# Kernel optimization log

Measured on AMD Instinct MI355X. Metric: run time of the kernel, lower is better.

The kernel has to match this reference:

```python
import jax, jax.numpy as jnp
import numpy as np

N_NODES = 50000
N_EDGES = 800000
IN_DIM = 128
HID = 32
HEADS = 8
N_CLASSES = 10
N_GRAPHS = 64
NEG_SLOPE = 0.2


def _lin(key, fan_in, fan_out):
    return jax.random.normal(key, (fan_in, fan_out), jnp.float32) / np.sqrt(fan_in)


def setup_inputs() -> dict:
    key = jax.random.key(0)
    ks = jax.random.split(key, 24)
    x = jax.random.normal(ks[0], (N_NODES, IN_DIM), jnp.float32)
    edge_index = jax.random.randint(ks[1], (2, N_EDGES), 0, N_NODES, jnp.int64)
    batch = jnp.sort(jax.random.randint(ks[2], (N_NODES,), 0, N_GRAPHS, jnp.int64))
    HC = HEADS * HID
    return {
        "x": x,
        "edge_index": edge_index,
        "batch": batch,
        # GATConv(IN_DIM, HID, heads=8): shared lin, att_src/att_dst, bias on concat output
        "gat_W": _lin(ks[3], IN_DIM, HC),
        "gat_att_src": jax.random.normal(ks[4], (HEADS, HID), jnp.float32) / np.sqrt(HID),
        "gat_att_dst": jax.random.normal(ks[5], (HEADS, HID), jnp.float32) / np.sqrt(HID),
        "gat_b": jnp.zeros((HC,), jnp.float32),
        # GraphConv(HC, HID): lin_rel (bias) on aggregated neighbors + lin_root (no bias)
        "W2_rel": _lin(ks[6], HC, HID), "b2": jnp.zeros((HID,), jnp.float32), "W2_root": _lin(ks[7], HC, HID),
        # SAGEConv(HID, HID): lin_l (bias) on mean-aggregated neighbors + lin_r (no bias)
        "W3_l": _lin(ks[8], HID, HID), "b3": jnp.zeros((HID,), jnp.float32), "W3_r": _lin(ks[9], HID, HID),
        # GraphConv(HID, HID)
        "W4_rel": _lin(ks[10], HID, HID), "b4": jnp.zeros((HID,), jnp.float32), "W4_root": _lin(ks[11], HID, HID),
        "fc1_W": _lin(ks[12], HID, HID), "fc1_b": jnp.zeros((HID,), jnp.float32),
        "fc2_W": _lin(ks[13], HID, N_CLASSES), "fc2_b": jnp.zeros((N_CLASSES,), jnp.float32),
    }


def _segment_softmax(logits, seg_ids, num_segments):
    # numerically-stable softmax over edges grouped by destination node
    m = jax.ops.segment_max(logits, seg_ids, num_segments=num_segments)
    e = jnp.exp(logits - m[seg_ids])
    z = jax.ops.segment_sum(e, seg_ids, num_segments=num_segments)
    return e / (z[seg_ids] + 1e-16)


def _gnn_forward(x, edge_index, batch, gat_W, gat_att_src, gat_att_dst, gat_b,
                 W2_rel, b2, W2_root, W3_l, b3, W3_r, W4_rel, b4, W4_root,
                 fc1_W, fc1_b, fc2_W, fc2_b):
    N = x.shape[0]
    src0, dst0 = edge_index[0], edge_index[1]

    # ---- GATConv (PyG defaults: add_self_loops=True, concat heads, neg_slope=0.2) ----
    loops = jnp.arange(N)
    src = jnp.concatenate([src0, loops])
    dst = jnp.concatenate([dst0, loops])
    h = (x @ gat_W).reshape(N, HEADS, HID)                 # [N,H,C]
    a_src = jnp.sum(h * gat_att_src, axis=-1)              # [N,H]
    a_dst = jnp.sum(h * gat_att_dst, axis=-1)              # [N,H]
    logits = jax.nn.leaky_relu(a_src[src] + a_dst[dst], NEG_SLOPE)  # [E',H]
    alpha = _segment_softmax(logits, dst, N)               # [E',H]
    msg = h[src] * alpha[:, :, None]                       # [E',H,C]
    out = jax.ops.segment_sum(msg, dst, num_segments=N).reshape(N, HEADS * HID) + gat_b
    x1 = jax.nn.relu(out)

    # ---- GraphConv (aggr='add'): lin_rel(sum_j x_j) + lin_root(x) ----
    agg = jax.ops.segment_sum(x1[src0], dst0, num_segments=N)
    x2 = jax.nn.relu(agg @ W2_rel + b2 + x1 @ W2_root)

    # ---- SAGEConv (aggr='mean'): lin_l(mean_j x_j) + lin_r(x) ----
    deg = jax.ops.segment_sum(jnp.ones((src0.shape[0],), x2.dtype), dst0, num_segments=N)
    agg = jax.ops.segment_sum(x2[src0], dst0, num_segments=N) / jnp.clip(deg, 1.0)[:, None]
    x3 = jax.nn.relu(agg @ W3_l + b3 + x2 @ W3_r)

    # ---- GraphConv ----
    agg = jax.ops.segment_sum(x3[src0], dst0, num_segments=N)
    x4 = jax.nn.relu(agg @ W4_rel + b4 + x3 @ W4_root)

    # ---- global_mean_pool + MLP head ----
    gsum = jax.ops.segment_sum(x4, batch, num_segments=N_GRAPHS)
    gcnt = jax.ops.segment_sum(jnp.ones((N,), x4.dtype), batch, num_segments=N_GRAPHS)
    g = gsum / jnp.clip(gcnt, 1.0)[:, None]                # [G,HID]
    g = jax.nn.relu(g @ fc1_W + fc1_b)
    return g @ fc2_W + fc2_b                               # [G, N_CLASSES]


def reference(x, edge_index, batch, gat_W, gat_att_src, gat_att_dst, gat_b,
              W2_rel, b2, W2_root, W3_l, b3, W3_r, W4_rel, b4, W4_root,
              fc1_W, fc1_b, fc2_W, fc2_b):
    return _gnn_forward(x, edge_index, batch, gat_W, gat_att_src, gat_att_dst, gat_b,
                        W2_rel, b2, W2_root, W3_l, b3, W3_r, W4_rel, b4, W4_root,
                        fc1_W, fc1_b, fc2_W, fc2_b)
```

## Files before the change

### kernel.cpp

```cpp
#include <hip/hip_runtime.h>

#define IN_DIM 128
#define HID 32
#define HEADS 8
#define HC 256
#define N_GRAPHS 64
#define N_CLASSES 10

#define SCAN_ELEMS 8
#define SCAN_BLOCK 256
#define SCAN_CHUNK (SCAN_ELEMS * SCAN_BLOCK)

typedef __attribute__((ext_vector_type(8))) short bf16x8;
typedef __attribute__((ext_vector_type(4))) float f32x4;

__device__ __forceinline__ float leaky(float v) { return v > 0.f ? v : 0.2f * v; }

__device__ __forceinline__ unsigned fenc(float f) {
    unsigned u = __float_as_uint(f);
    return (u & 0x80000000u) ? ~u : (u | 0x80000000u);
}
__device__ __forceinline__ float fdec(unsigned u) {
    return __uint_as_float((u & 0x80000000u) ? (u & 0x7FFFFFFFu) : ~u);
}
__device__ __forceinline__ unsigned short bf16r(float f) {
    unsigned u = __float_as_uint(f);
    return (unsigned short)((u + 0x7FFFu + ((u >> 16) & 1u)) >> 16);
}
__device__ __forceinline__ float bdec(unsigned short u) {
    return __uint_as_float(((unsigned)u) << 16);
}

__global__ __launch_bounds__(256) void k_setup(
    int* __restrict__ deg, int N, unsigned* __restrict__ gm,
    float* __restrict__ gsum, float* __restrict__ gcnt, int* __restrict__ counter,
    const float* __restrict__ W, const float* __restrict__ Wrel, const float* __restrict__ Wroot,
    unsigned short* __restrict__ Wb, unsigned short* __restrict__ W2b)
{
    int i = blockIdx.x * 256 + threadIdx.x;
    if (i < N) deg[i] = 0;
    if (i < HEADS) gm[i] = 0u;
    if (i < N_GRAPHS * HID) gsum[i] = 0.f;
    if (i < N_GRAPHS) gcnt[i] = 0.f;
    if (i == 0) *counter = 0;

    if (blockIdx.x < 16) {
        int slot = blockIdx.x * 256 + threadIdx.x;
        int lane = slot & 63;
        int ctg  = (slot >> 6) & 15;
        int ks   = slot >> 10;
        int col  = ctg * 16 + (lane & 15);
        int kb   = ks * 32 + (lane >> 4) * 8;
        unsigned short t[8];
#pragma unroll
        for (int j = 0; j < 8; ++j) t[j] = bf16r(W[(size_t)(kb + j) * HC + col]);
        ushort4* dst = (ushort4*)(Wb + (size_t)slot * 8);
        dst[0] = make_ushort4(t[0], t[1], t[2], t[3]);
        dst[1] = make_ushort4(t[4], t[5], t[6], t[7]);
    } else if (blockIdx.x < 24) {
        int slot = (blockIdx.x - 16) * 256 + threadIdx.x;
        int lane = slot & 63;
        int ct   = (slot >> 6) & 3;
        int ks   = slot >> 8;
        int col  = ct * 16 + (lane & 15);
        int kb   = ks * 32 + (lane >> 4) * 8;
        const float* src = (col < HID) ? (Wrel + col) : (Wroot + (col - HID));
        unsigned short t[8];
#pragma unroll
        for (int j = 0; j < 8; ++j) t[j] = bf16r(src[(size_t)(kb + j) * HID]);
        ushort4* dst = (ushort4*)(W2b + (size_t)slot * 8);
        dst[0] = make_ushort4(t[0], t[1], t[2], t[3]);
        dst[1] = make_ushort4(t[4], t[5], t[6], t[7]);
    }
}

__global__ __launch_bounds__(256) void k_gemm_deg(
    const float* __restrict__ x, const unsigned short* __restrict__ Wb,
    const float* __restrict__ att_s, const float* __restrict__ att_d,
    unsigned short* __restrict__ h, float* __restrict__ a_src, float* __restrict__ a_dst, int N,
    const int* __restrict__ edst, int* __restrict__ deg, unsigned short* __restrict__ rank,
    int E, int gemmBlocks)
{
    if (blockIdx.x >= gemmBlocks) {
        int i = (blockIdx.x - gemmBlocks) * 256 + threadIdx.x;
        if (i < E) rank[i] = (unsigned short)atomicAdd(&deg[edst[i]], 1);
        return;
    }
    int w = threadIdx.x >> 6;
    int lane = threadIdx.x & 63;
    int lrow = lane & 15, lgrp = lane >> 4;
    int nb = blockIdx.x * 16;

    int rowc = min(nb + lrow, N - 1);
    const float* xrow = x + (size_t)rowc * IN_DIM + lgrp * 8;

    f32x4 acc0 = {0.f, 0.f, 0.f, 0.f}, acc1 = acc0, acc2 = acc0, acc3 = acc0;

#pragma unroll
    for (int ks = 0; ks < 4; ++ks) {
        float4 a0 = *(const float4*)(xrow + ks * 32);
        float4 a1 = *(const float4*)(xrow + ks * 32 + 4);
        bf16x8 af;
        af[0] = (short)bf16r(a0.x); af[1] = (short)bf16r(a0.y);
        af[2] = (short)bf16r(a0.z); af[3] = (short)bf16r(a0.w);
        af[4] = (short)bf16r(a1.x); af[5] = (short)bf16r(a1.y);
        af[6] = (short)bf16r(a1.z); af[7] = (short)bf16r(a1.w);
        const bf16x8* bp = (const bf16x8*)(Wb + ((size_t)(ks * 16 + w * 4) * 64 + lane) * 8);
        acc0 = __builtin_amdgcn_mfma_f32_16x16x32_bf16(af, bp[0 * 64], acc0, 0, 0, 0);
        acc1 = __builtin_amdgcn_mfma_f32_16x16x32_bf16(af, bp[1 * 64], acc1, 0, 0, 0);
        acc2 = __builtin_amdgcn_mfma_f32_16x16x32_bf16(af, bp[2 * 64], acc2, 0, 0, 0);
        acc3 = __builtin_amdgcn_mfma_f32_16x16x32_bf16(af, bp[3 * 64], acc3, 0, 0, 0);
    }

    int cbase = w * 64;
#pragma unroll
    for (int r = 0; r < 4; ++r) {
        int n = nb + lgrp * 4 + r;
        if (n < N) {
            unsigned short* hp = h + (size_t)n * HC + cbase + lrow;
            hp[0]  = bf16r(acc0[r]);
            hp[16] = bf16r(acc1[r]);
            hp[32] = bf16r(acc2[r]);
            hp[48] = bf16r(acc3[r]);
        }
    }
    int h0 = cbase >> 5, h1 = h0 + 1;
    float as00 = att_s[h0 * HID + lrow], as01 = att_s[h0 * HID + 16 + lrow];
    float as10 = att_s[h1 * HID + lrow], as11 = att_s[h1 * HID + 16 + lrow];
    float ad00 = att_d[h0 * HID + lrow], ad01 = att_d[h0 * HID + 16 + lrow];
    float ad10 = att_d[h1 * HID + lrow], ad11 = att_d[h1 * HID + 16 + lrow];
#pragma unroll
    for (int r = 0; r < 4; ++r) {
        float ps0 = acc0[r] * as00 + acc1[r] * as01;
        float pd0 = acc0[r] * ad00 + acc1[r] * ad01;
        float ps1 = acc2[r] * as10 + acc3[r] * as11;
        float pd1 = acc2[r] * ad10 + acc3[r] * ad11;
#pragma unroll
        for (int d = 1; d < 16; d <<= 1) {
            ps0 += __shfl_xor(ps0, d); pd0 += __shfl_xor(pd0, d);
            ps1 += __shfl_xor(ps1, d); pd1 += __shfl_xor(pd1, d);
        }
        int n = nb + lgrp * 4 + r;
        if (lrow == 0 && n < N) {
            a_src[n * HEADS + h0] = ps0; a_dst[n * HEADS + h0] = pd0;
            a_src[n * HEADS + h1] = ps1; a_dst[n * HEADS + h1] = pd1;
        }
    }
}

__global__ __launch_bounds__(256) void k_amax_scan(
    const float* __restrict__ asrc, unsigned* __restrict__ gm, int N,
    const int* __restrict__ deg, int* __restrict__ bsum, int amaxBlocks)
{
    int tid = threadIdx.x;
    if (blockIdx.x < amaxBlocks) {
        __shared__ float sm[4][HEADS];
        float m[HEADS];
#pragma unroll
        for (int hh = 0; hh < HEADS; ++hh) m[hh] = -1e30f;
        int stride = amaxBlocks * 256;
        for (int n = blockIdx.x * 256 + tid; n < N; n += stride) {
#pragma unroll
            for (int hh = 0; hh < HEADS; ++hh) m[hh] = fmaxf(m[hh], asrc[n * HEADS + hh]);
        }
#pragma unroll
        for (int hh = 0; hh < HEADS; ++hh)
            for (int d = 1; d < 64; d <<= 1) m[hh] = fmaxf(m[hh], __shfl_xor(m[hh], d));
        int lane = tid & 63, wv = tid >> 6;
        if (lane == 0)
#pragma unroll
            for (int hh = 0; hh < HEADS; ++hh) sm[wv][hh] = m[hh];
        __syncthreads();
        if (tid == 0) {
#pragma unroll
            for (int hh = 0; hh < HEADS; ++hh) {
                float mm = fmaxf(fmaxf(sm[0][hh], sm[1][hh]), fmaxf(sm[2][hh], sm[3][hh]));
                atomicMax(&gm[hh], fenc(mm));
            }
        }
    } else {
        int bid = blockIdx.x - amaxBlocks;
        int base = bid * SCAN_CHUNK + tid * SCAN_ELEMS;
        int s = 0;
#pragma unroll
        for (int i = 0; i < SCAN_ELEMS; ++i) { int idx = base + i; if (idx < N) s += deg[idx]; }
#pragma unroll
        for (int d = 1; d < 64; d <<= 1) s += __shfl_xor(s, d);
        __shared__ int ws[4];
        int lane = tid & 63, wv = tid >> 6;
        if (lane == 0) ws[wv] = s;
        __syncthreads();
        if (tid == 0) bsum[bid] = ws[0] + ws[1] + ws[2] + ws[3];
    }
}

__global__ __launch_bounds__(SCAN_BLOCK) void k_scan_write(
    const int* __restrict__ deg, const int* __restrict__ bsum,
    int* __restrict__ off, int N)
{
    __shared__ int sbpre;
    if (threadIdx.x == 0) {
        int s = 0;
        for (int b = 0; b < blockIdx.x; ++b) s += bsum[b];
        sbpre = s;
    }
    int base = blockIdx.x * SCAN_CHUNK + threadIdx.x * SCAN_ELEMS;
    int dl[SCAN_ELEMS];
    int s = 0;
#pragma unroll
    for (int i = 0; i < SCAN_ELEMS; ++i) {
        int idx = base + i;
        dl[i] = (idx < N) ? deg[idx] : 0;
        s += dl[i];
    }
    int lane = threadIdx.x & 63, wv = threadIdx.x >> 6;
    int v = s;
#pragma unroll
    for (int d = 1; d < 64; d <<= 1) { int t = __shfl_up(v, d); if (lane >= d) v += t; }
    __shared__ int ws[4];
    if (lane == 63) ws[wv] = v;
    __syncthreads();
    int wadd = 0;
    for (int w = 0; w < wv; ++w) wadd += ws[w];
    int run = sbpre + wadd + (v - s);
#pragma unroll
    for (int i = 0; i < SCAN_ELEMS; ++i) {
        int idx = base + i;
        if (idx < N) {
            off[idx] = run;
            run += dl[i];
            if (idx == N - 1) off[N] = run;
        }
    }
}

__global__ void k_scatter(const int* __restrict__ src, const int* __restrict__ dst,
                          const unsigned short* __restrict__ rank, const int* __restrict__ off,
                          unsigned short* __restrict__ srcs, int E) {
    int i = blockIdx.x * blockDim.x + threadIdx.x;
    if (i < E) srcs[off[dst[i]] + (int)rank[i]] = (unsigned short)src[i];
}

__global__ __launch_bounds__(256) void k_gat(
    const unsigned short* __restrict__ h, const float* __restrict__ asrc, const float* __restrict__ adst,
    const float* __restrict__ bias, const int* __restrict__ off, const unsigned short* __restrict__ srcs,
    const unsigned* __restrict__ gm, unsigned short* __restrict__ x1, int N)
{
    int v = (blockIdx.x * blockDim.x + threadIdx.x) >> 6;
    int lane = threadIdx.x & 63;
    if (v >= N) return;
    int head = lane >> 3;
    float ad = adst[v * HEADS + head];
    float asv = asrc[v * HEADS + head];
    float m = leaky(fdec(gm[head]) + ad);
    int beg = off[v], end = off[v + 1];

    ushort4 hv = *(const ushort4*)(h + (size_t)v * HC + lane * 4);
    float w = __expf(leaky(asv + ad) - m);
    float z = w;
    float acc0 = w * bdec(hv.x), acc1 = w * bdec(hv.y), acc2 = w * bdec(hv.z), acc3 = w * bdec(hv.w);

    int e = beg;
    for (; e + 4 <= end; e += 4) {
        int s0 = srcs[e + 0], s1 = srcs[e + 1], s2 = srcs[e + 2], s3 = srcs[e + 3];
        float l0 = asrc[s0 * HEADS + head], l1 = asrc[s1 * HEADS + head];
        float l2 = asrc[s2 * HEADS + head], l3 = asrc[s3 * HEADS + head];
        ushort4 h0 = *(const ushort4*)(h + (size_t)s0 * HC + lane * 4);
        ushort4 h1 = *(const ushort4*)(h + (size_t)s1 * HC + lane * 4);
        ushort4 h2 = *(const ushort4*)(h + (size_t)s2 * HC + lane * 4);
        ushort4 h3 = *(const ushort4*)(h + (size_t)s3 * HC + lane * 4);
        float w0 = __expf(leaky(l0 + ad) - m);
        float w1 = __expf(leaky(l1 + ad) - m);
        float w2 = __expf(leaky(l2 + ad) - m);
        float w3 = __expf(leaky(l3 + ad) - m);
        z += (w0 + w1) + (w2 + w3);
        acc0 += w0 * bdec(h0.x) + w1 * bdec(h1.x) + w2 * bdec(h2.x) + w3 * bdec(h3.x);
        acc1 += w0 * bdec(h0.y) + w1 * bdec(h1.y) + w2 * bdec(h2.y) + w3 * bdec(h3.y);
        acc2 += w0 * bdec(h0.z) + w1 * bdec(h1.z) + w2 * bdec(h2.z) + w3 * bdec(h3.z);
        acc3 += w0 * bdec(h0.w) + w1 * bdec(h1.w) + w2 * bdec(h2.w) + w3 * bdec(h3.w);
    }
    for (; e < end; ++e) {
        int s = srcs[e];
        float we = __expf(leaky(asrc[s * HEADS + head] + ad) - m);
        ushort4 hs = *(const ushort4*)(h + (size_t)s * HC + lane * 4);
        z += we;
        acc0 += we * bdec(hs.x); acc1 += we * bdec(hs.y);
        acc2 += we * bdec(hs.z); acc3 += we * bdec(hs.w);
    }
    float inv_z = 1.f / (z + 1e-16f);
    int c = lane * 4;
    float4 b4 = *(const float4*)(bias + c);
    ushort4 o;
    o.x = bf16r(fmaxf(acc0 * inv_z + b4.x, 0.f));
    o.y = bf16r(fmaxf(acc1 * inv_z + b4.y, 0.f));
    o.z = bf16r(fmaxf(acc2 * inv_z + b4.z, 0.f));
    o.w = bf16r(fmaxf(acc3 * inv_z + b4.w, 0.f));
    *(ushort4*)(x1 + (size_t)v * HC + c) = o;
}

__global__ __launch_bounds__(256) void k_zr2(
    const unsigned short* __restrict__ x1b, const unsigned short* __restrict__ W2b,
    unsigned short* __restrict__ z, float* __restrict__ r, int N)
{
    int w = threadIdx.x >> 6;
    int lane = threadIdx.x & 63;
    int lrow = lane & 15, lgrp = lane >> 4;
    int nb = blockIdx.x * 16;
    int rowc = min(nb + lrow, N - 1);
    const unsigned short* xrow = x1b + (size_t)rowc * HC + lgrp * 8;

    f32x4 acc = {0.f, 0.f, 0.f, 0.f};
#pragma unroll
    for (int ks = 0; ks < 8; ++ks) {
        bf16x8 af = *(const bf16x8*)(xrow + ks * 32);
        const bf16x8* bp = (const bf16x8*)(W2b + ((size_t)(ks * 4 + w) * 64 + lane) * 8);
        acc = __builtin_amdgcn_mfma_f32_16x16x32_bf16(af, *bp, acc, 0, 0, 0);
    }
    int col = w * 16 + lrow;
#pragma unroll
    for (int rr = 0; rr < 4; ++rr) {
        int n = nb + lgrp * 4 + rr;
        if (n < N) {
            if (col < HID) z[(size_t)n * HID + col] = bf16r(acc[rr]);
            else           r[(size_t)n * HID + (col - HID)] = acc[rr];
        }
    }
}

__global__ __launch_bounds__(256) void k_agg_lin(
    const unsigned short* __restrict__ z, const float* __restrict__ r, const float* __restrict__ b,
    const int* __restrict__ off, const unsigned short* __restrict__ srcs,
    unsigned short* __restrict__ xout, int N)
{
    int nl = threadIdx.x >> 5, j = threadIdx.x & 31;
    int n = blockIdx.x * 8 + nl;
    if (n >= N) return;
    float acc = r[n * HID + j] + b[j];
    int beg = off[n], end = off[n + 1];
    int e = beg;
    for (; e + 4 <= end; e += 4) {
        int s0 = srcs[e], s1 = srcs[e + 1], s2 = srcs[e + 2], s3 = srcs[e + 3];
        float v0 = bdec(z[s0 * HID + j]);
        float v1 = bdec(z[s1 * HID + j]);
        float v2 = bdec(z[s2 * HID + j]);
        float v3 = bdec(z[s3 * HID + j]);
        acc += (v0 + v1) + (v2 + v3);
    }
    for (; e < end; ++e)
        acc += bdec(z[srcs[e] * HID + j]);
    xout[n * HID + j] = bf16r(fmaxf(acc, 0.f));
}

template <bool MEAN>
__global__ __launch_bounds__(256) void k_conv32(
    const unsigned short* __restrict__ xin, const int* __restrict__ off, const unsigned short* __restrict__ srcs,
    const float* __restrict__ Wl, const float* __restrict__ Wr, const float* __restrict__ b,
    unsigned short* __restrict__ xout, int N)
{
    __shared__ float sagg[8][HID];
    __shared__ float sx[8][HID];
    int nl = threadIdx.x >> 5, j = threadIdx.x & 31;
    int n = blockIdx.x * 8 + nl;
    int nc = min(n, N - 1);
    int beg = off[nc], end = off[nc + 1];
    float acc = 0.f;
    int e = beg;
    for (; e + 4 <= end; e += 4) {
        int s0 = srcs[e], s1 = srcs[e + 1], s2 = srcs[e + 2], s3 = srcs[e + 3];
        float v0 = bdec(xin[s0 * HID + j]);
        float v1 = bdec(xin[s1 * HID + j]);
        float v2 = bdec(xin[s2 * HID + j]);
        float v3 = bdec(xin[s3 * HID + j]);
        acc += (v0 + v1) + (v2 + v3);
    }
    for (; e < end; ++e)
        acc += bdec(xin[srcs[e] * HID + j]);
    if (MEAN) acc /= fmaxf((float)(end - beg), 1.f);
    sagg[nl][j] = acc;
    sx[nl][j] = bdec(xin[nc * HID + j]);
    __syncthreads();
    float o = b[j];
#pragma unroll
    for (int k = 0; k < HID; ++k)
        o += sagg[nl][k] * Wl[k * HID + j] + sx[nl][k] * Wr[k * HID + j];
    o = fmaxf(o, 0.f);
    if (n < N) xout[n * HID + j] = bf16r(o);
}

__global__ __launch_bounds__(256) void k_pool_head(
    const unsigned short* __restrict__ x4, const int* __restrict__ batch,
    float* __restrict__ gsum, float* __restrict__ gcnt, int N, int* __restrict__ counter,
    const float* __restrict__ fc1W, const float* __restrict__ fc1b,
    const float* __restrict__ fc2W, const float* __restrict__ fc2b,
    float* __restrict__ out)
{
    const int PER_BLOCK = 1024;
    int base = blockIdx.x * PER_BLOCK;
    int endn = min(base + PER_BLOCK, N);
    int c = threadIdx.x & 31, no = threadIdx.x >> 5;
    {
        float acc = 0.f, cnt = 0.f;
        int curg = -1;
        for (int n = base + no; n < endn; n += 8) {
            int g = batch[n];
            if (g != curg) {
                if (curg >= 0) {
                    atomicAdd(&gsum[curg * HID + c], acc);
                    if (c == 0) atomicAdd(&gcnt[curg], cnt);
                }
                curg = g; acc = 0.f; cnt = 0.f;
            }
            acc += bdec(x4[n * HID + c]);
            cnt += 1.f;
        }
        if (curg >= 0) {
            atomicAdd(&gsum[curg * HID + c], acc);
            if (c == 0) atomicAdd(&gcnt[curg], cnt);
        }
    }
    __threadfence();
    __shared__ int lastFlag;
    if (threadIdx.x == 0) lastFlag = (atomicAdd(counter, 1) == (int)gridDim.x - 1);
    __syncthreads();
    if (!lastFlag) return;

    __shared__ float g[N_GRAPHS * HID];
    __shared__ float t[N_GRAPHS * HID];
    __shared__ float gc[N_GRAPHS];
    int tid = threadIdx.x;
    if (tid < N_GRAPHS) gc[tid] = atomicAdd(&gcnt[tid], 0.f);
    __syncthreads();
    for (int i = tid; i < N_GRAPHS * HID; i += 256)
        g[i] = atomicAdd(&gsum[i], 0.f) / fmaxf(gc[i >> 5], 1.f);
    __syncthreads();
    for (int i = tid; i < N_GRAPHS * HID; i += 256) {
        int gi = i >> 5, j = i & 31;
        float o = fc1b[j];
#pragma unroll
        for (int k = 0; k < HID; ++k) o += g[gi * HID + k] * fc1W[k * HID + j];
        t[i] = fmaxf(o, 0.f);
    }
    __syncthreads();
    for (int i = tid; i < N_GRAPHS * N_CLASSES; i += 256) {
        int gi = i / N_CLASSES, j = i % N_CLASSES;
        float o = fc2b[j];
#pragma unroll
        for (int k = 0; k < HID; ++k) o += t[gi * HID + k] * fc2W[k * N_CLASSES + j];
        out[i] = o;
    }
}

extern "C" void kernel_launch(void* const* d_in, const int* in_sizes, int n_in,
                              void* d_out, int out_size, void* d_ws, size_t ws_size,
                              hipStream_t stream)
{
    const float* x       = (const float*)d_in[0];
    const int*   eidx    = (const int*)d_in[1];
    const int*   batch   = (const int*)d_in[2];
    const float* gat_W   = (const float*)d_in[3];
    const float* att_s   = (const float*)d_in[4];
    const float* att_d   = (const float*)d_in[5];
    const float* gat_b   = (const float*)d_in[6];
    const float* W2_rel  = (const float*)d_in[7];
    const float* b2      = (const float*)d_in[8];
    const float* W2_root = (const float*)d_in[9];
    const float* W3_l    = (const float*)d_in[10];
    const float* b3      = (const float*)d_in[11];
    const float* W3_r    = (const float*)d_in[12];
    const float* W4_rel  = (const float*)d_in[13];
    const float* b4      = (const float*)d_in[14];
    const float* W4_root = (const float*)d_in[15];
    const float* fc1_W   = (const float*)d_in[16];
    const float* fc1_b   = (const float*)d_in[17];
    const float* fc2_W   = (const float*)d_in[18];
    const float* fc2_b   = (const float*)d_in[19];

    const int N = in_sizes[2];
    const int E = in_sizes[1] / 2;
    const int* esrc = eidx;
    const int* edst = eidx + E;

    char* wsb = (char*)d_ws;
    size_t ofs = 0;
    auto alloc = [&](size_t bytes) {
        char* p = wsb + ofs;
        ofs = (ofs + bytes + 255) & ~(size_t)255;
        return p;
    };
    unsigned short* h   = (unsigned short*)alloc((size_t)N * HC * 2);
    unsigned short* Wb  = (unsigned short*)alloc((size_t)IN_DIM * HC * 2);
    unsigned short* W2b = (unsigned short*)alloc((size_t)HC * 64 * 2);
    unsigned short* x1b = (unsigned short*)alloc((size_t)N * HC * 2);
    float* a_src = (float*)alloc((size_t)N * HEADS * 4);
    float* a_dst = (float*)alloc((size_t)N * HEADS * 4);
    int*   deg   = (int*)alloc((size_t)N * 4);
    int*   off   = (int*)alloc((size_t)(N + 1) * 4);
    unsigned short* rank = (unsigned short*)alloc((size_t)E * 2);
    unsigned short* srcs = (unsigned short*)alloc((size_t)E * 2);
    int*   bsum  = (int*)alloc((size_t)128 * 4);
    unsigned short* zb  = (unsigned short*)alloc((size_t)N * HID * 2);
    float* r     = (float*)alloc((size_t)N * HID * 4);
    unsigned short* x2b = (unsigned short*)alloc((size_t)N * HID * 2);
    unsigned short* x3b = (unsigned short*)alloc((size_t)N * HID * 2);
    unsigned short* x4b = (unsigned short*)alloc((size_t)N * HID * 2);
    float* gsum  = (float*)alloc(N_GRAPHS * HID * 4);
    float* gcnt  = (float*)alloc(N_GRAPHS * 4);
    unsigned* gm = (unsigned*)alloc(HEADS * 4);
    int*  counter = (int*)alloc(4);
    (void)ws_size; (void)n_in; (void)out_size;

    const int nscan = (N + SCAN_CHUNK - 1) / SCAN_CHUNK;
    const int gemmBlocks = (N + 15) / 16;
    const int degBlocks  = (E + 255) / 256;
    const int amaxBlocks = 32;
    const int poolBlocks = (N + 1023) / 1024;

    k_setup<<<(N + 255) / 256, 256, 0, stream>>>(deg, N, gm, gsum, gcnt, counter,
                                                 gat_W, W2_rel, W2_root, Wb, W2b);
    k_gemm_deg<<<gemmBlocks + degBlocks, 256, 0, stream>>>(
        x, Wb, att_s, att_d, h, a_src, a_dst, N, edst, deg, rank, E, gemmBlocks);
    k_amax_scan<<<amaxBlocks + nscan, 256, 0, stream>>>(a_src, gm, N, deg, bsum, amaxBlocks);
    k_scan_write<<<nscan, SCAN_BLOCK, 0, stream>>>(deg, bsum, off, N);
    k_scatter<<<(E + 255) / 256, 256, 0, stream>>>(esrc, edst, rank, off, srcs, E);
    k_gat<<<(N + 3) / 4, 256, 0, stream>>>(h, a_src, a_dst, gat_b, off, srcs, gm, x1b, N);
    k_zr2<<<(N + 15) / 16, 256, 0, stream>>>(x1b, W2b, zb, r, N);
    k_agg_lin<<<(N + 7) / 8, 256, 0, stream>>>(zb, r, b2, off, srcs, x2b, N);
    k_conv32<true><<<(N + 7) / 8, 256, 0, stream>>>(x2b, off, srcs, W3_l, W3_r, b3, x3b, N);
    k_conv32<false><<<(N + 7) / 8, 256, 0, stream>>>(x3b, off, srcs, W4_rel, W4_root, b4, x4b, N);
    k_pool_head<<<poolBlocks, 256, 0, stream>>>(x4b, batch, gsum, gcnt, N, counter,
                                                fc1_W, fc1_b, fc2_W, fc2_b, (float*)d_out);
}
```

Measured before the change: 309.2 us.

## Vectorize amax loads, warp-scan block prefix, unroll GAT gather by eight, split GAT launch

```diff
diff --git a/kernel.cpp b/kernel.cpp
--- a/kernel.cpp
+++ b/kernel.cpp
@@ -160,8 +160,12 @@
         for (int hh = 0; hh < HEADS; ++hh) m[hh] = -1e30f;
         int stride = amaxBlocks * 256;
         for (int n = blockIdx.x * 256 + tid; n < N; n += stride) {
-#pragma unroll
-            for (int hh = 0; hh < HEADS; ++hh) m[hh] = fmaxf(m[hh], asrc[n * HEADS + hh]);
+            float4 p0 = *(const float4*)(asrc + (size_t)n * HEADS);
+            float4 p1 = *(const float4*)(asrc + (size_t)n * HEADS + 4);
+            m[0] = fmaxf(m[0], p0.x); m[1] = fmaxf(m[1], p0.y);
+            m[2] = fmaxf(m[2], p0.z); m[3] = fmaxf(m[3], p0.w);
+            m[4] = fmaxf(m[4], p1.x); m[5] = fmaxf(m[5], p1.y);
+            m[6] = fmaxf(m[6], p1.z); m[7] = fmaxf(m[7], p1.w);
         }
 #pragma unroll
         for (int hh = 0; hh < HEADS; ++hh)
@@ -199,10 +203,11 @@
     int* __restrict__ off, int N)
 {
     __shared__ int sbpre;
-    if (threadIdx.x == 0) {
-        int s = 0;
-        for (int b = 0; b < blockIdx.x; ++b) s += bsum[b];
-        sbpre = s;
+    if (threadIdx.x < 64) {
+        int lane = threadIdx.x;
+        int bv = (lane < (int)blockIdx.x) ? bsum[lane] : 0;
+        for (int d = 1; d < 64; d <<= 1) { int t = __shfl_up(bv, d); if (lane >= d) bv += t; }
+        if (lane == 63) sbpre = bv;
     }
     int base = blockIdx.x * SCAN_CHUNK + threadIdx.x * SCAN_ELEMS;
     int dl[SCAN_ELEMS];
@@ -244,11 +249,11 @@
 __global__ __launch_bounds__(256) void k_gat(
     const unsigned short* __restrict__ h, const float* __restrict__ asrc, const float* __restrict__ adst,
     const float* __restrict__ bias, const int* __restrict__ off, const unsigned short* __restrict__ srcs,
-    const unsigned* __restrict__ gm, unsigned short* __restrict__ x1, int N)
-{
-    int v = (blockIdx.x * blockDim.x + threadIdx.x) >> 6;
+    const unsigned* __restrict__ gm, unsigned short* __restrict__ x1, int n0, int n1)
+{
+    int v = n0 + ((blockIdx.x * blockDim.x + threadIdx.x) >> 6);
     int lane = threadIdx.x & 63;
-    if (v >= N) return;
+    if (v >= n1) return;
     int head = lane >> 3;
     float ad = adst[v * HEADS + head];
     float asv = asrc[v * HEADS + head];
@@ -261,23 +266,50 @@
     float acc0 = w * bdec(hv.x), acc1 = w * bdec(hv.y), acc2 = w * bdec(hv.z), acc3 = w * bdec(hv.w);
 
     int e = beg;
+    for (; e + 8 <= end; e += 8) {
+        int s0 = srcs[e + 0], s1 = srcs[e + 1], s2 = srcs[e + 2], s3 = srcs[e + 3];
+        int s4 = srcs[e + 4], s5 = srcs[e + 5], s6 = srcs[e + 6], s7 = srcs[e + 7];
+        float l0 = asrc[s0 * HEADS + head], l1 = asrc[s1 * HEADS + head];
+        float l2 = asrc[s2 * HEADS + head], l3 = asrc[s3 * HEADS + head];
+        float l4 = asrc[s4 * HEADS + head], l5 = asrc[s5 * HEADS + head];
+        float l6 = asrc[s6 * HEADS + head], l7 = asrc[s7 * HEADS + head];
+        ushort4 g0 = *(const ushort4*)(h + (size_t)s0 * HC + lane * 4);
+        ushort4 g1 = *(const ushort4*)(h + (size_t)s1 * HC + lane * 4);
+        ushort4 g2 = *(const ushort4*)(h + (size_t)s2 * HC + lane * 4);
+        ushort4 g3 = *(const ushort4*)(h + (size_t)s3 * HC + lane * 4);
+        ushort4 g4 = *(const ushort4*)(h + (size_t)s4 * HC + lane * 4);
+        ushort4 g5 = *(const ushort4*)(h + (size_t)s5 * HC + lane * 4);
+        ushort4 g6 = *(const ushort4*)(h + (size_t)s6 * HC + lane * 4);
+        ushort4 g7 = *(const ushort4*)(h + (size_t)s7 * HC + lane * 4);
+        float w0 = __expf(leaky(l0 + ad) - m), w1 = __expf(leaky(l1 + ad) - m);
+        float w2 = __expf(leaky(l2 + ad) - m), w3 = __expf(leaky(l3 + ad) - m);
+        float w4 = __expf(leaky(l4 + ad) - m), w5 = __expf(leaky(l5 + ad) - m);
+        float w6 = __expf(leaky(l6 + ad) - m), w7 = __expf(leaky(l7 + ad) - m);
+        z += ((w0 + w1) + (w2 + w3)) + ((w4 + w5) + (w6 + w7));
+        acc0 += (w0 * bdec(g0.x) + w1 * bdec(g1.x) + w2 * bdec(g2.x) + w3 * bdec(g3.x))
+              + (w4 * bdec(g4.x) + w5 * bdec(g5.x) + w6 * bdec(g6.x) + w7 * bdec(g7.x));
+        acc1 += (w0 * bdec(g0.y) + w1 * bdec(g1.y) + w2 * bdec(g2.y) + w3 * bdec(g3.y))
+              + (w4 * bdec(g4.y) + w5 * bdec(g5.y) + w6 * bdec(g6.y) + w7 * bdec(g7.y));
+        acc2 += (w0 * bdec(g0.z) + w1 * bdec(g1.z) + w2 * bdec(g2.z) + w3 * bdec(g3.z))
+              + (w4 * bdec(g4.z) + w5 * bdec(g5.z) + w6 * bdec(g6.z) + w7 * bdec(g7.z));
+        acc3 += (w0 * bdec(g0.w) + w1 * bdec(g1.w) + w2 * bdec(g2.w) + w3 * bdec(g3.w))
+              + (w4 * bdec(g4.w) + w5 * bdec(g5.w) + w6 * bdec(g6.w) + w7 * bdec(g7.w));
+    }
     for (; e + 4 <= end; e += 4) {
         int s0 = srcs[e + 0], s1 = srcs[e + 1], s2 = srcs[e + 2], s3 = srcs[e + 3];
         float l0 = asrc[s0 * HEADS + head], l1 = asrc[s1 * HEADS + head];
         float l2 = asrc[s2 * HEADS + head], l3 = asrc[s3 * HEADS + head];
-        ushort4 h0 = *(const ushort4*)(h + (size_t)s0 * HC + lane * 4);
-        ushort4 h1 = *(const ushort4*)(h + (size_t)s1 * HC + lane * 4);
-        ushort4 h2 = *(const ushort4*)(h + (size_t)s2 * HC + lane * 4);
-        ushort4 h3 = *(const ushort4*)(h + (size_t)s3 * HC + lane * 4);
-        float w0 = __expf(leaky(l0 + ad) - m);
-        float w1 = __expf(leaky(l1 + ad) - m);
-        float w2 = __expf(leaky(l2 + ad) - m);
-        float w3 = __expf(leaky(l3 + ad) - m);
+        ushort4 g0 = *(const ushort4*)(h + (size_t)s0 * HC + lane * 4);
+        ushort4 g1 = *(const ushort4*)(h + (size_t)s1 * HC + lane * 4);
+        ushort4 g2 = *(const ushort4*)(h + (size_t)s2 * HC + lane * 4);
+        ushort4 g3 = *(const ushort4*)(h + (size_t)s3 * HC + lane * 4);
+        float w0 = __expf(leaky(l0 + ad) - m), w1 = __expf(leaky(l1 + ad) - m);
+        float w2 = __expf(leaky(l2 + ad) - m), w3 = __expf(leaky(l3 + ad) - m);
         z += (w0 + w1) + (w2 + w3);
-        acc0 += w0 * bdec(h0.x) + w1 * bdec(h1.x) + w2 * bdec(h2.x) + w3 * bdec(h3.x);
-        acc1 += w0 * bdec(h0.y) + w1 * bdec(h1.y) + w2 * bdec(h2.y) + w3 * bdec(h3.y);
-        acc2 += w0 * bdec(h0.z) + w1 * bdec(h1.z) + w2 * bdec(h2.z) + w3 * bdec(h3.z);
-        acc3 += w0 * bdec(h0.w) + w1 * bdec(h1.w) + w2 * bdec(h2.w) + w3 * bdec(h3.w);
+        acc0 += w0 * bdec(g0.x) + w1 * bdec(g1.x) + w2 * bdec(g2.x) + w3 * bdec(g3.x);
+        acc1 += w0 * bdec(g0.y) + w1 * bdec(g1.y) + w2 * bdec(g2.y) + w3 * bdec(g3.y);
+        acc2 += w0 * bdec(g0.z) + w1 * bdec(g1.z) + w2 * bdec(g2.z) + w3 * bdec(g3.z);
+        acc3 += w0 * bdec(g0.w) + w1 * bdec(g1.w) + w2 * bdec(g2.w) + w3 * bdec(g3.w);
     }
     for (; e < end; ++e) {
         int s = srcs[e];
@@ -512,8 +544,9 @@
     const int nscan = (N + SCAN_CHUNK - 1) / SCAN_CHUNK;
     const int gemmBlocks = (N + 15) / 16;
     const int degBlocks  = (E + 255) / 256;
-    const int amaxBlocks = 32;
+    const int amaxBlocks = 128;
     const int poolBlocks = (N + 1023) / 1024;
+    const int nhalf = (N + 1) / 2;
 
     k_setup<<<(N + 255) / 256, 256, 0, stream>>>(deg, N, gm, gsum, gcnt, counter,
                                                  gat_W, W2_rel, W2_root, Wb, W2b);
@@ -522,7 +555,8 @@
     k_amax_scan<<<amaxBlocks + nscan, 256, 0, stream>>>(a_src, gm, N, deg, bsum, amaxBlocks);
     k_scan_write<<<nscan, SCAN_BLOCK, 0, stream>>>(deg, bsum, off, N);
     k_scatter<<<(E + 255) / 256, 256, 0, stream>>>(esrc, edst, rank, off, srcs, E);
-    k_gat<<<(N + 3) / 4, 256, 0, stream>>>(h, a_src, a_dst, gat_b, off, srcs, gm, x1b, N);
+    k_gat<<<(nhalf + 3) / 4, 256, 0, stream>>>(h, a_src, a_dst, gat_b, off, srcs, gm, x1b, 0, nhalf);
+    k_gat<<<(N - nhalf + 3) / 4, 256, 0, stream>>>(h, a_src, a_dst, gat_b, off, srcs, gm, x1b, nhalf, N);
     k_zr2<<<(N + 15) / 16, 256, 0, stream>>>(x1b, W2b, zb, r, N);
     k_agg_lin<<<(N + 7) / 8, 256, 0, stream>>>(zb, r, b2, off, srcs, x2b, N);
     k_conv32<true><<<(N + 7) / 8, 256, 0, stream>>>(x2b, off, srcs, W3_l, W3_r, b3, x3b, N);
```

Result: slower. 323.0 us (+4.5%).

## Stage GEMM output via LDS, vectorize amax loads, parallelize block prefix, raise pool/amax blocks

Applied to the files above, without the earlier changes.

```diff
diff --git a/kernel.cpp b/kernel.cpp
--- a/kernel.cpp
+++ b/kernel.cpp
@@ -81,6 +81,7 @@
     const int* __restrict__ edst, int* __restrict__ deg, unsigned short* __restrict__ rank,
     int E, int gemmBlocks)
 {
+    __shared__ unsigned short sh[4][16][72];
     if (blockIdx.x >= gemmBlocks) {
         int i = (blockIdx.x - gemmBlocks) * 256 + threadIdx.x;
         if (i < E) rank[i] = (unsigned short)atomicAdd(&deg[edst[i]], 1);
@@ -115,13 +116,20 @@
     int cbase = w * 64;
 #pragma unroll
     for (int r = 0; r < 4; ++r) {
-        int n = nb + lgrp * 4 + r;
+        int lr = lgrp * 4 + r;
+        sh[w][lr][lrow]      = bf16r(acc0[r]);
+        sh[w][lr][16 + lrow] = bf16r(acc1[r]);
+        sh[w][lr][32 + lrow] = bf16r(acc2[r]);
+        sh[w][lr][48 + lrow] = bf16r(acc3[r]);
+    }
+#pragma unroll
+    for (int round = 0; round < 2; ++round) {
+        int row = (lane >> 3) + round * 8;
+        int chunk = lane & 7;
+        int n = nb + row;
         if (n < N) {
-            unsigned short* hp = h + (size_t)n * HC + cbase + lrow;
-            hp[0]  = bf16r(acc0[r]);
-            hp[16] = bf16r(acc1[r]);
-            hp[32] = bf16r(acc2[r]);
-            hp[48] = bf16r(acc3[r]);
+            uint4 t = *(const uint4*)(&sh[w][row][chunk * 8]);
+            *(uint4*)(h + (size_t)n * HC + cbase + chunk * 8) = t;
         }
     }
     int h0 = cbase >> 5, h1 = h0 + 1;
@@ -160,8 +168,12 @@
         for (int hh = 0; hh < HEADS; ++hh) m[hh] = -1e30f;
         int stride = amaxBlocks * 256;
         for (int n = blockIdx.x * 256 + tid; n < N; n += stride) {
-#pragma unroll
-            for (int hh = 0; hh < HEADS; ++hh) m[hh] = fmaxf(m[hh], asrc[n * HEADS + hh]);
+            float4 p0 = *(const float4*)(asrc + (size_t)n * HEADS);
+            float4 p1 = *(const float4*)(asrc + (size_t)n * HEADS + 4);
+            m[0] = fmaxf(m[0], p0.x); m[1] = fmaxf(m[1], p0.y);
+            m[2] = fmaxf(m[2], p0.z); m[3] = fmaxf(m[3], p0.w);
+            m[4] = fmaxf(m[4], p1.x); m[5] = fmaxf(m[5], p1.y);
+            m[6] = fmaxf(m[6], p1.z); m[7] = fmaxf(m[7], p1.w);
         }
 #pragma unroll
         for (int hh = 0; hh < HEADS; ++hh)
@@ -199,10 +211,11 @@
     int* __restrict__ off, int N)
 {
     __shared__ int sbpre;
-    if (threadIdx.x == 0) {
-        int s = 0;
-        for (int b = 0; b < blockIdx.x; ++b) s += bsum[b];
-        sbpre = s;
+    if (threadIdx.x < 64) {
+        int lane = threadIdx.x;
+        int bv = (lane < (int)blockIdx.x) ? bsum[lane] : 0;
+        for (int d = 1; d < 64; d <<= 1) { int t = __shfl_up(bv, d); if (lane >= d) bv += t; }
+        if (lane == 63) sbpre = bv;
     }
     int base = blockIdx.x * SCAN_CHUNK + threadIdx.x * SCAN_ELEMS;
     int dl[SCAN_ELEMS];
@@ -394,7 +407,7 @@
     const float* __restrict__ fc2W, const float* __restrict__ fc2b,
     float* __restrict__ out)
 {
-    const int PER_BLOCK = 1024;
+    const int PER_BLOCK = 128;
     int base = blockIdx.x * PER_BLOCK;
     int endn = min(base + PER_BLOCK, N);
     int c = threadIdx.x & 31, no = threadIdx.x >> 5;
@@ -512,8 +525,8 @@
     const int nscan = (N + SCAN_CHUNK - 1) / SCAN_CHUNK;
     const int gemmBlocks = (N + 15) / 16;
     const int degBlocks  = (E + 255) / 256;
-    const int amaxBlocks = 32;
-    const int poolBlocks = (N + 1023) / 1024;
+    const int amaxBlocks = 128;
+    const int poolBlocks = (N + 127) / 128;
 
     k_setup<<<(N + 255) / 256, 256, 0, stream>>>(deg, N, gm, gsum, gcnt, counter,
                                                  gat_W, W2_rel, W2_root, Wb, W2b);
```

After: 303.9 us. No clear change (-1.7%).
